# Optimization experiments

Measured on AMD Instinct MI355X. Metric: run time of the kernel, lower is better.

## Reference

```python
import jax, jax.numpy as jnp
import numpy as np

POOL = 7
IMG_H, IMG_W = 1024, 1024
EPS = 1e-3  # keras BatchNormalization default epsilon


def crop_and_resize(fmap, boxes, ph, pw):
    # TF tf.image.crop_and_resize (bilinear), box_indices == batch index of each roi.
    # fmap: [B,H,W,C], boxes: [B,N,4] normalized (y1,x1,y2,x2) -> [B,N,ph,pw,C]
    B, H, W, C = fmap.shape
    y1, x1, y2, x2 = jnp.split(boxes, 4, axis=-1)  # each [B,N,1]
    fy = jnp.arange(ph, dtype=boxes.dtype) / (ph - 1)
    fx = jnp.arange(pw, dtype=boxes.dtype) / (pw - 1)
    ys = (y1 + (y2 - y1) * fy) * (H - 1)  # [B,N,ph]
    xs = (x1 + (x2 - x1) * fx) * (W - 1)  # [B,N,pw]
    y0 = jnp.floor(ys)
    x0 = jnp.floor(xs)
    wy = (ys - y0)[:, :, :, None, None]  # [B,N,ph,1,1]
    wx = (xs - x0)[:, :, None, :, None]  # [B,N,1,pw,1]
    y0i = jnp.clip(y0.astype(jnp.int32), 0, H - 1)
    y1i = jnp.clip(y0i + 1, 0, H - 1)
    x0i = jnp.clip(x0.astype(jnp.int32), 0, W - 1)
    x1i = jnp.clip(x0i + 1, 0, W - 1)
    b = jnp.arange(B)[:, None, None, None]
    yi0 = y0i[:, :, :, None]; yi1 = y1i[:, :, :, None]   # [B,N,ph,1]
    xi0 = x0i[:, :, None, :]; xi1 = x1i[:, :, None, :]   # [B,N,1,pw]
    v00 = fmap[b, yi0, xi0]  # [B,N,ph,pw,C]
    v01 = fmap[b, yi0, xi1]
    v10 = fmap[b, yi1, xi0]
    v11 = fmap[b, yi1, xi1]
    top = v00 + (v01 - v00) * wx
    bot = v10 + (v11 - v10) * wx
    return top + (bot - top) * wy


def pyramid_roi_align(rois, fmaps, pool):
    # rois are stop-gradient in the original layer
    rois = jax.lax.stop_gradient(rois)
    y1, x1, y2, x2 = jnp.split(rois, 4, axis=-1)
    h = y2 - y1
    w = x2 - x1
    scale = 256.0 / np.sqrt(float(IMG_H * IMG_W))
    lvl = jnp.log2(jnp.maximum(jnp.sqrt(h * w), 1e-9) / scale)
    lvl = jnp.clip(4 + jnp.round(lvl).astype(jnp.int32), 2, 5)[..., 0]  # [B,N]
    B, N = rois.shape[:2]
    C = fmaps[0].shape[-1]
    out = jnp.zeros((B, N, pool, pool, C), fmaps[0].dtype)
    for i, fm in enumerate(fmaps):  # levels 2..5, fixed small loop
        sel = (lvl == i + 2)[:, :, None, None, None]
        out = jnp.where(sel, crop_and_resize(fm, rois, pool, pool), out)
    return out


def bn_train(x, gamma, beta):
    # keras BatchNorm with training=True: biased batch stats over all axes but channel
    m = x.mean(axis=(0, 1))
    v = x.var(axis=(0, 1))
    return (x - m) * jax.lax.rsqrt(v + EPS) * gamma + beta


def setup_inputs() -> dict:
    key = jax.random.key(0)
    ks = jax.random.split(key, 12)
    B, N, C, F = 2, 1000, 256, 1024
    # rois: valid boxes, sizes spanning all pyramid levels
    tl = jax.random.uniform(ks[0], (B, N, 2), jnp.float32, 0.0, 0.6)
    sz = jax.random.uniform(ks[1], (B, N, 2), jnp.float32, 0.02, 0.4)
    br = jnp.minimum(tl + sz, 1.0)
    rois = jnp.concatenate([tl[..., :1], tl[..., 1:], br[..., :1], br[..., 1:]], axis=-1)
    s = 0.02
    return {
        "rois": rois,
        "p2": jax.random.normal(ks[2], (B, 256, 256, C), jnp.float32),
        "p3": jax.random.normal(ks[3], (B, 128, 128, C), jnp.float32),
        "p4": jax.random.normal(ks[4], (B, 64, 64, C), jnp.float32),
        "p5": jax.random.normal(ks[5], (B, 32, 32, C), jnp.float32),
        "conv1_w": jax.random.normal(ks[6], (POOL, POOL, C, F), jnp.float32) * s,
        "conv1_b": jnp.zeros((F,), jnp.float32),
        "bn1_g": jnp.ones((F,), jnp.float32),
        "bn1_b": jnp.zeros((F,), jnp.float32),
        "conv2_w": jax.random.normal(ks[7], (F, F), jnp.float32) * s,
        "conv2_b": jnp.zeros((F,), jnp.float32),
        "bn2_g": jnp.ones((F,), jnp.float32),
        "bn2_b": jnp.zeros((F,), jnp.float32),
        "cls_w": jax.random.normal(ks[8], (F, 2), jnp.float32) * s,
        "cls_b": jnp.zeros((2,), jnp.float32),
        "delta_w": jax.random.normal(ks[9], (F, 8), jnp.float32) * s,
        "delta_b": jnp.zeros((8,), jnp.float32),
    }


def reference(rois, p2, p3, p4, p5, conv1_w, conv1_b, bn1_g, bn1_b,
              conv2_w, conv2_b, bn2_g, bn2_b, cls_w, cls_b, delta_w, delta_b):
    B, N = rois.shape[:2]
    n_classes = cls_w.shape[-1]
    pooled = pyramid_roi_align(rois, (p2, p3, p4, p5), POOL)  # [B,N,7,7,C]
    # Conv2D(F,(7,7),'valid') on a 7x7 input == full contraction over (h,w,c)
    x = jnp.einsum('bnhwc,hwcf->bnf', pooled, conv1_w) + conv1_b
    x = jax.nn.relu(bn_train(x, bn1_g, bn1_b))
    x = x @ conv2_w + conv2_b  # 1x1 conv == dense
    shared = jax.nn.relu(bn_train(x, bn2_g, bn2_b))  # [B,N,F]
    logits = shared @ cls_w + cls_b                  # [B,N,n_classes]
    probs = jax.nn.softmax(logits, axis=-1)
    deltas = (shared @ delta_w + delta_b).reshape(B, N, n_classes, 4)
    return logits, probs, deltas
```

## Files before the change

### kernel.cpp

```cpp
#include <hip/hip_runtime.h>
#include <hip/hip_bf16.h>

#define NB     2
#define NROI   1000
#define CIN    256
#define FDIM   1024
#define M_ROWS 2000
#define K1     12544
#define EPSBN  1e-3f
#define MN     (M_ROWS * FDIM)

typedef short bf16x8 __attribute__((ext_vector_type(8)));
typedef short bf16x4 __attribute__((ext_vector_type(4)));
typedef float f32x4  __attribute__((ext_vector_type(4)));

__device__ __forceinline__ void gld_lds16(const void* g, void* l) {
  __builtin_amdgcn_global_load_lds((const __attribute__((address_space(1))) char*)g,
                                   (__attribute__((address_space(3))) char*)l, 16, 0, 0);
}

__global__ __launch_bounds__(256) void transpose_to_bf16_v2(const float* __restrict__ W,
                                                            __hip_bfloat16* __restrict__ WT,
                                                            int K, int N) {
  __shared__ float tt[64][129];
  int k0 = blockIdx.x * 128, n0 = blockIdx.y * 64;
  int t = threadIdx.x;
  int r = t >> 4, cg = t & 15;
#pragma unroll
  for (int i = 0; i < 8; i++) {
    int row = i * 16 + r;
    f32x4 v = *(const f32x4*)(W + (size_t)(k0 + row) * N + n0 + cg * 4);
#pragma unroll
    for (int j = 0; j < 4; j++) tt[cg * 4 + j][row] = v[j];
  }
  __syncthreads();
  int n = t >> 4, g = t & 15;
#pragma unroll
  for (int pp = 0; pp < 4; pp++) {
    int nn = pp * 16 + n;
    bf16x8 o;
#pragma unroll
    for (int i = 0; i < 8; i++) {
      __hip_bfloat16 hh = __float2bfloat16(tt[nn][g * 8 + i]);
      o[i] = *reinterpret_cast<short*>(&hh);
    }
    *(bf16x8*)((short*)WT + (size_t)(n0 + nn) * K + k0 + g * 8) = o;
  }
}

__global__ __launch_bounds__(256) void roi_align_v2(const float* __restrict__ rois,
                                                    const float* __restrict__ p2,
                                                    const float* __restrict__ p3,
                                                    const float* __restrict__ p4,
                                                    const float* __restrict__ p5,
                                                    __hip_bfloat16* __restrict__ pooled) {
  int rn = blockIdx.x;
  int b = rn / NROI;

  const float* roi = rois + (size_t)rn * 4;
  float y1 = roi[0], x1 = roi[1], y2 = roi[2], x2 = roi[3];
  float h = y2 - y1, w = x2 - x1;
  float lvl = log2f(fmaxf(sqrtf(h * w), 1e-9f) * 4.0f);
  int li = 4 + (int)rintf(lvl);
  li = min(max(li, 2), 5) - 2;

  const float* fm; int H;
  switch (li) {
    case 0:  fm = p2; H = 256; break;
    case 1:  fm = p3; H = 128; break;
    case 2:  fm = p4; H = 64;  break;
    default: fm = p5; H = 32;  break;
  }
  int W = H;
  const float* fb = fm + (size_t)b * H * W * CIN;

  int lane = threadIdx.x & 63, wv = threadIdx.x >> 6;
  int c4 = lane * 4;

  for (int pos = wv; pos < 49; pos += 4) {
    int py = pos / 7, px = pos - py * 7;
    float fy = (float)py / 6.0f, fx = (float)px / 6.0f;
    float ys = (y1 + (y2 - y1) * fy) * (float)(H - 1);
    float xs = (x1 + (x2 - x1) * fx) * (float)(W - 1);
    float y0f = floorf(ys), x0f = floorf(xs);
    float wy = ys - y0f, wx = xs - x0f;
    int y0 = min(max((int)y0f, 0), H - 1);
    int x0 = min(max((int)x0f, 0), W - 1);
    int y1i = min(y0 + 1, H - 1);
    int x1i = min(x0 + 1, W - 1);

    f32x4 v00 = *(const f32x4*)(fb + ((size_t)y0 * W + x0) * CIN + c4);
    f32x4 v01 = *(const f32x4*)(fb + ((size_t)y0 * W + x1i) * CIN + c4);
    f32x4 v10 = *(const f32x4*)(fb + ((size_t)y1i * W + x0) * CIN + c4);
    f32x4 v11 = *(const f32x4*)(fb + ((size_t)y1i * W + x1i) * CIN + c4);

    f32x4 top = v00 + (v01 - v00) * wx;
    f32x4 bot = v10 + (v11 - v10) * wx;
    f32x4 val = top + (bot - top) * wy;

    bf16x4 o;
#pragma unroll
    for (int j = 0; j < 4; j++) {
      __hip_bfloat16 hh = __float2bfloat16(val[j]);
      o[j] = *reinterpret_cast<short*>(&hh);
    }
    *(bf16x4*)((short*)pooled + ((size_t)rn * 49 + pos) * CIN + c4) = o;
  }
}

template<int KSLICES>
__global__ __launch_bounds__(512) void gemm8w(const short* __restrict__ A,
                                              const short* __restrict__ BT,
                                              float* __restrict__ P,
                                              int M, int N, int K) {
  __shared__ short As[4 * 128 * 32];
  __shared__ short Bs[4 * 256 * 32];

  int nwg = gridDim.x;
  int bid = blockIdx.x;
  int cpx = nwg >> 3;
  int wg = (bid & 7) * cpx + (bid >> 3);

  int MT = (M + 127) >> 7;
  int NTn = N >> 8;
  int tiles = MT * NTn;
  int ks = wg / tiles;
  int rem = wg % tiles;
  int tm = rem % MT, tn = rem / MT;
  int m0 = tm * 128, n0 = tn * 256;
  int Kc = K / KSLICES;
  int NT = Kc >> 6;
  size_t kb = (size_t)ks * Kc;

  int tid = threadIdx.x;
  int lane = tid & 63, wid = tid >> 6;
  int wr = wid >> 2, wc = wid & 3;

  int srow = tid >> 2;
  int g = (tid & 3) ^ (srow & 3);
  const short* Agb  = A  + (size_t)min(m0 + srow, M - 1) * K + kb + g * 8;
  const short* Bgb0 = BT + (size_t)(n0 + srow) * K + kb + g * 8;
  const short* Bgb1 = Bgb0 + (size_t)128 * K;
  int aoff  = wid * 512;
  int boff0 = wid * 512;
  int boff1 = 4096 + wid * 512;

  int lr = lane & 15;
  int slotoff = ((lane >> 4) ^ (lane & 3)) * 8;
  const short* Ard = As + (wr * 64 + lr) * 32 + slotoff;
  const short* Brd = Bs + (wc * 64 + lr) * 32 + slotoff;

  f32x4 acc[4][4] = {};

#define STAGE(s) do {                                                        \
    int ts_ = (s) >> 1, kh_ = (s) & 1, b_ = ts_ & 1;                         \
    int ko_ = ts_ * 64 + kh_ * 32;                                           \
    short* Ad_ = (short*)As + (b_ * 2 + kh_) * 4096 + aoff;                  \
    short* Bd_ = (short*)Bs + (b_ * 2 + kh_) * 8192;                         \
    gld_lds16(Agb + ko_, Ad_);                                               \
    gld_lds16(Bgb0 + ko_, Bd_ + boff0);                                      \
    gld_lds16(Bgb1 + ko_, Bd_ + boff1);                                      \
  } while (0)

  STAGE(0); STAGE(1); STAGE(2);

  for (int t = 0; t < NT; ++t) {
    int b = t & 1;
#pragma unroll
    for (int kh = 0; kh < 2; ++kh) {
      __builtin_amdgcn_sched_barrier(0);
      if (t < NT - 1)      asm volatile("s_waitcnt vmcnt(6)" ::: "memory");
      else if (kh == 0)    asm volatile("s_waitcnt vmcnt(3)" ::: "memory");
      else                 asm volatile("s_waitcnt vmcnt(0)" ::: "memory");
      __builtin_amdgcn_s_barrier();
      __builtin_amdgcn_sched_barrier(0);

      const short* Ab = Ard + (b * 2 + kh) * 4096;
      const short* Bb = Brd + (b * 2 + kh) * 8192;
      bf16x8 af[4], bf_[4];
#pragma unroll
      for (int mi = 0; mi < 4; mi++) af[mi] = *(const bf16x8*)(Ab + mi * 512);
#pragma unroll
      for (int ni = 0; ni < 4; ni++) bf_[ni] = *(const bf16x8*)(Bb + ni * 512);

      if (kh == 0) { if (t + 1 < NT) STAGE(2 * t + 3); }
      else         { if (t + 2 < NT) STAGE(2 * t + 4); }

      __builtin_amdgcn_sched_barrier(0);
      asm volatile("s_waitcnt lgkmcnt(0)" ::: "memory");
      __builtin_amdgcn_sched_barrier(0);
      __builtin_amdgcn_s_setprio(1);
#pragma unroll
      for (int mi = 0; mi < 4; mi++)
#pragma unroll
        for (int ni = 0; ni < 4; ni++)
          acc[mi][ni] = __builtin_amdgcn_mfma_f32_16x16x32_bf16(af[mi], bf_[ni], acc[mi][ni], 0, 0, 0);
      __builtin_amdgcn_s_setprio(0);
    }
  }
#undef STAGE

  float* Pb = P + (size_t)ks * M * N;
  int crow = (lane >> 4) * 4, ccol = lane & 15;
#pragma unroll
  for (int mi = 0; mi < 4; mi++) {
    int rb = m0 + wr * 64 + mi * 16 + crow;
#pragma unroll
    for (int ni = 0; ni < 4; ni++) {
      int col = n0 + wc * 64 + ni * 16 + ccol;
#pragma unroll
      for (int r = 0; r < 4; r++) {
        int row = rb + r;
        if (row < M) Pb[(size_t)row * N + col] = acc[mi][ni][r];
      }
    }
  }
}

template<int KSLICES>
__global__ __launch_bounds__(256) void gemm128(const short* __restrict__ A,
                                               const short* __restrict__ BT,
                                               float* __restrict__ P,
                                               int M, int N, int K) {
  __shared__ short As[128 * 32];
  __shared__ short Bs[128 * 32];
  int nwg = gridDim.x;
  int bid = blockIdx.x;
  int cpx = nwg >> 3;
  int wg = (bid & 7) * cpx + (bid >> 3);

  int MT = (M + 127) >> 7;
  int NT = N >> 7;
  int ks   = wg / (MT * NT);
  int tile = wg % (MT * NT);
  int tm = tile % MT, tn = tile / MT;
  int m0 = tm * 128, n0 = tn * 128;
  int Kc = K / KSLICES;
  int kb = ks * Kc;

  int t = threadIdx.x;
  int lane = t & 63, wid = t >> 6;
  int wr = wid >> 1, wc = wid & 1;

  int q0 = wid * 64 + lane;
  int q1 = 256 + q0;
  int as0 = (q0 & 3) * 8, as1 = (q1 & 3) * 8;
  int ar0 = min(m0 + (q0 >> 2), M - 1);
  int ar1 = min(m0 + (q1 >> 2), M - 1);
  const short* Ag0 = A + (size_t)ar0 * K + kb + as0;
  const short* Ag1 = A + (size_t)ar1 * K + kb + as1;
  const short* Bg0 = BT + (size_t)(n0 + (q0 >> 2)) * K + kb + as0;
  const short* Bg1 = BT + (size_t)(n0 + (q1 >> 2)) * K + kb + as1;
  short* Asb0 = As + wid * 512;
  short* Asb1 = As + 2048 + wid * 512;
  short* Bsb0 = Bs + wid * 512;
  short* Bsb1 = Bs + 2048 + wid * 512;

  int lrow = lane & 15, lk = (lane >> 4) * 8;
  const short* Ar = As + (wr * 64 + lrow) * 32 + lk;
  const short* Br = Bs + (wc * 64 + lrow) * 32 + lk;

  f32x4 acc[4][4] = {};

  for (int k0 = 0; k0 < Kc; k0 += 32) {
    __syncthreads();
    gld_lds16(Ag0 + k0, Asb0);
    gld_lds16(Ag1 + k0, Asb1);
    gld_lds16(Bg0 + k0, Bsb0);
    gld_lds16(Bg1 + k0, Bsb1);
    __syncthreads();

    bf16x8 af[4], bfr[4];
#pragma unroll
    for (int i = 0; i < 4; i++) {
      af[i]  = *(const bf16x8*)(Ar + i * 512);
      bfr[i] = *(const bf16x8*)(Br + i * 512);
    }
#pragma unroll
    for (int mi = 0; mi < 4; mi++)
#pragma unroll
      for (int ni = 0; ni < 4; ni++)
        acc[mi][ni] = __builtin_amdgcn_mfma_f32_16x16x32_bf16(af[mi], bfr[ni], acc[mi][ni], 0, 0, 0);
  }

  float* Pb = P + (size_t)ks * M * N;
  int crow = (lane >> 4) * 4, ccol = lane & 15;
#pragma unroll
  for (int mi = 0; mi < 4; mi++) {
    int rb = m0 + wr * 64 + mi * 16 + crow;
#pragma unroll
    for (int ni = 0; ni < 4; ni++) {
      int col = n0 + wc * 64 + ni * 16 + ccol;
#pragma unroll
      for (int r = 0; r < 4; r++) {
        int row = rb + r;
        if (row < M) Pb[(size_t)row * N + col] = acc[mi][ni][r];
      }
    }
  }
}

__global__ void reduce_bias_stats(const float* __restrict__ P, const float* __restrict__ bias,
                                  float* __restrict__ X, float* __restrict__ stats,
                                  int M, int KS) {
  int t = threadIdx.x;
  int col = t * 4;
  f32x4 bv = *(const f32x4*)(bias + col);
  f32x4 s = {0, 0, 0, 0}, q = {0, 0, 0, 0};
  for (int r = blockIdx.x; r < M; r += gridDim.x) {
    size_t base = (size_t)r * FDIM + col;
    f32x4 v = *(const f32x4*)(P + base);
    for (int c = 1; c < KS; c++)
      v = v + *(const f32x4*)(P + (size_t)c * MN + base);
    v = v + bv;
    *(f32x4*)(X + base) = v;
    s = s + v;
    q = q + v * v;
  }
#pragma unroll
  for (int j = 0; j < 4; j++) {
    atomicAdd(&stats[col + j], s[j]);
    atomicAdd(&stats[FDIM + col + j], q[j]);
  }
}

__global__ void bn_norm_relu_bf16(const float* __restrict__ X, const float* __restrict__ stats,
                                  const float* __restrict__ g, const float* __restrict__ bta,
                                  __hip_bfloat16* __restrict__ obf, int M) {
  int idx = blockIdx.x * blockDim.x + threadIdx.x;
  if (idx >= M * FDIM) return;
  int f = idx & (FDIM - 1);
  float inv_m = 1.0f / (float)M;
  float mean = stats[f] * inv_m;
  float var = stats[FDIM + f] * inv_m - mean * mean;
  float xn = (X[idx] - mean) * rsqrtf(var + EPSBN) * g[f] + bta[f];
  obf[idx] = __float2bfloat16(fmaxf(xn, 0.0f));
}

__global__ void heads_bn(const float* __restrict__ X2, const float* __restrict__ stats,
                         const float* __restrict__ gg, const float* __restrict__ bb,
                         const float* __restrict__ cls_w, const float* __restrict__ cls_b,
                         const float* __restrict__ dw, const float* __restrict__ db,
                         float* __restrict__ out) {
  int row = blockIdx.x * 4 + (threadIdx.x >> 6);
  int lane = threadIdx.x & 63;
  if (row >= M_ROWS) return;
  const float* xrow = X2 + (size_t)row * FDIM;
  float inv_m = 1.0f / (float)M_ROWS;
  float a[10];
#pragma unroll
  for (int j = 0; j < 10; j++) a[j] = 0.0f;
  for (int k = lane; k < FDIM; k += 64) {
    float mean = stats[k] * inv_m;
    float var = stats[FDIM + k] * inv_m - mean * mean;
    float v = fmaxf((xrow[k] - mean) * rsqrtf(var + EPSBN) * gg[k] + bb[k], 0.0f);
    a[0] += v * cls_w[k * 2 + 0];
    a[1] += v * cls_w[k * 2 + 1];
#pragma unroll
    for (int j = 0; j < 8; j++) a[2 + j] += v * dw[k * 8 + j];
  }
#pragma unroll
  for (int j = 0; j < 10; j++)
    for (int o = 32; o > 0; o >>= 1) a[j] += __shfl_xor(a[j], o, 64);
  if (lane == 0) {
    float l0 = a[0] + cls_b[0], l1 = a[1] + cls_b[1];
    out[row * 2 + 0] = l0;
    out[row * 2 + 1] = l1;
    float mx = fmaxf(l0, l1);
    float e0 = expf(l0 - mx), e1 = expf(l1 - mx);
    float inv = 1.0f / (e0 + e1);
    out[4000 + row * 2 + 0] = e0 * inv;
    out[4000 + row * 2 + 1] = e1 * inv;
#pragma unroll
    for (int j = 0; j < 8; j++) out[8000 + row * 8 + j] = a[2 + j] + db[j];
  }
}

extern "C" void kernel_launch(void* const* d_in, const int* in_sizes, int n_in,
                              void* d_out, int out_size, void* d_ws, size_t ws_size,
                              hipStream_t stream) {
  const float* rois    = (const float*)d_in[0];
  const float* p2      = (const float*)d_in[1];
  const float* p3      = (const float*)d_in[2];
  const float* p4      = (const float*)d_in[3];
  const float* p5      = (const float*)d_in[4];
  const float* conv1_w = (const float*)d_in[5];
  const float* conv1_b = (const float*)d_in[6];
  const float* bn1_g   = (const float*)d_in[7];
  const float* bn1_b   = (const float*)d_in[8];
  const float* conv2_w = (const float*)d_in[9];
  const float* conv2_b = (const float*)d_in[10];
  const float* bn2_g   = (const float*)d_in[11];
  const float* bn2_b   = (const float*)d_in[12];
  const float* cls_w   = (const float*)d_in[13];
  const float* cls_b   = (const float*)d_in[14];
  const float* delta_w = (const float*)d_in[15];
  const float* delta_b = (const float*)d_in[16];
  float* out = (float*)d_out;

  char* ws = (char*)d_ws;
  size_t off = 0;
  __hip_bfloat16* pooled = (__hip_bfloat16*)(ws + off); off += (size_t)M_ROWS * K1 * 2;
  __hip_bfloat16* w1t    = (__hip_bfloat16*)(ws + off); off += (size_t)K1 * FDIM * 2;
  float* stats1          = (float*)(ws + off);          off += 2 * FDIM * 4;
  float* stats2          = (float*)(ws + off);          off += 2 * FDIM * 4;
  char*  Preg            = ws + off;                    off += (size_t)5 * MN * 4;
  float* part1           = (float*)Preg;
  float* x1              = (float*)Preg;
  __hip_bfloat16* x1n    = (__hip_bfloat16*)(Preg + (size_t)MN * 4);
  __hip_bfloat16* w2t    = (__hip_bfloat16*)(Preg + (size_t)2 * MN * 4);
  float* part2           = (float*)(Preg + (size_t)3 * MN * 4);
  float* x2              = part2;

  hipMemsetAsync(stats1, 0, 4 * FDIM * sizeof(float), stream);

  transpose_to_bf16_v2<<<dim3(K1 / 128, FDIM / 64), 256, 0, stream>>>(conv1_w, w1t, K1, FDIM);

  roi_align_v2<<<M_ROWS, 256, 0, stream>>>(rois, p2, p3, p4, p5, pooled);

  gemm8w<4><<<256, 512, 0, stream>>>((const short*)pooled, (const short*)w1t, part1,
                                     M_ROWS, FDIM, K1);
  reduce_bias_stats<<<256, 256, 0, stream>>>(part1, conv1_b, x1, stats1, M_ROWS, 4);

  bn_norm_relu_bf16<<<(MN + 255) / 256, 256, 0, stream>>>(x1, stats1, bn1_g, bn1_b, x1n, M_ROWS);

  transpose_to_bf16_v2<<<dim3(FDIM / 128, FDIM / 64), 256, 0, stream>>>(conv2_w, (__hip_bfloat16*)w2t, FDIM, FDIM);

  gemm128<2><<<256, 256, 0, stream>>>((const short*)x1n, (const short*)w2t, part2,
                                      M_ROWS, FDIM, FDIM);
  reduce_bias_stats<<<256, 256, 0, stream>>>(part2, conv2_b, x2, stats2, M_ROWS, 2);

  heads_bn<<<(M_ROWS + 3) / 4, 256, 0, stream>>>(x2, stats2, bn2_g, bn2_b,
                                                 cls_w, cls_b, delta_w, delta_b, out);

  (void)in_sizes; (void)n_in; (void)out_size; (void)ws_size;
}
```

Before: 217.1 us.

## Fuse prep kernels into one launch and reuse gemm8w for second GEMM

```diff
diff --git a/kernel.cpp b/kernel.cpp
--- a/kernel.cpp
+++ b/kernel.cpp
@@ -19,92 +19,112 @@
                                    (__attribute__((address_space(3))) char*)l, 16, 0, 0);
 }
 
-__global__ __launch_bounds__(256) void transpose_to_bf16_v2(const float* __restrict__ W,
-                                                            __hip_bfloat16* __restrict__ WT,
-                                                            int K, int N) {
-  __shared__ float tt[64][129];
-  int k0 = blockIdx.x * 128, n0 = blockIdx.y * 64;
+__global__ __launch_bounds__(256) void prep_kernel(
+    const float* __restrict__ rois,
+    const float* __restrict__ p2, const float* __restrict__ p3,
+    const float* __restrict__ p4, const float* __restrict__ p5,
+    __hip_bfloat16* __restrict__ pooled,
+    const float* __restrict__ conv1_w, __hip_bfloat16* __restrict__ w1t,
+    const float* __restrict__ conv2_w, __hip_bfloat16* __restrict__ w2t,
+    float* __restrict__ stats) {
+  __shared__ float tt[64][65];
+  int idx = blockIdx.x;
   int t = threadIdx.x;
-  int r = t >> 4, cg = t & 15;
-#pragma unroll
-  for (int i = 0; i < 8; i++) {
-    int row = i * 16 + r;
-    f32x4 v = *(const f32x4*)(W + (size_t)(k0 + row) * N + n0 + cg * 4);
-#pragma unroll
-    for (int j = 0; j < 4; j++) tt[cg * 4 + j][row] = v[j];
+
+  if (idx == 0) {
+#pragma unroll
+    for (int i = 0; i < 4; i++)
+      ((f32x4*)stats)[t + i * 256] = f32x4{0, 0, 0, 0};
+    return;
+  }
+
+  if (idx < 1 + M_ROWS) {
+    int rn = idx - 1;
+    int b = rn / NROI;
+
+    const float* roi = rois + (size_t)rn * 4;
+    float y1 = roi[0], x1 = roi[1], y2 = roi[2], x2 = roi[3];
+    float h = y2 - y1, w = x2 - x1;
+    float lvl = log2f(fmaxf(sqrtf(h * w), 1e-9f) * 4.0f);
+    int li = 4 + (int)rintf(lvl);
+    li = min(max(li, 2), 5) - 2;
+
+    const float* fm; int H;
+    switch (li) {
+      case 0:  fm = p2; H = 256; break;
+      case 1:  fm = p3; H = 128; break;
+      case 2:  fm = p4; H = 64;  break;
+      default: fm = p5; H = 32;  break;
+    }
+    int W = H;
+    const float* fb = fm + (size_t)b * H * W * CIN;
+
+    int lane = t & 63, wv = t >> 6;
+    int c4 = lane * 4;
+
+    for (int pos = wv; pos < 49; pos += 4) {
+      int py = pos / 7, px = pos - py * 7;
+      float fy = (float)py / 6.0f, fx = (float)px / 6.0f;
+      float ys = (y1 + (y2 - y1) * fy) * (float)(H - 1);
+      float xs = (x1 + (x2 - x1) * fx) * (float)(W - 1);
+      float y0f = floorf(ys), x0f = floorf(xs);
+      float wy = ys - y0f, wx = xs - x0f;
+      int y0 = min(max((int)y0f, 0), H - 1);
+      int x0 = min(max((int)x0f, 0), W - 1);
+      int y1i = min(y0 + 1, H - 1);
+      int x1i = min(x0 + 1, W - 1);
+
+      f32x4 v00 = *(const f32x4*)(fb + ((size_t)y0 * W + x0) * CIN + c4);
+      f32x4 v01 = *(const f32x4*)(fb + ((size_t)y0 * W + x1i) * CIN + c4);
+      f32x4 v10 = *(const f32x4*)(fb + ((size_t)y1i * W + x0) * CIN + c4);
+      f32x4 v11 = *(const f32x4*)(fb + ((size_t)y1i * W + x1i) * CIN + c4);
+
+      f32x4 top = v00 + (v01 - v00) * wx;
+      f32x4 bot = v10 + (v11 - v10) * wx;
+      f32x4 val = top + (bot - top) * wy;
+
+      bf16x4 o;
+#pragma unroll
+      for (int j = 0; j < 4; j++) {
+        __hip_bfloat16 hh = __float2bfloat16(val[j]);
+        o[j] = *reinterpret_cast<short*>(&hh);
+      }
+      *(bf16x4*)((short*)pooled + ((size_t)rn * 49 + pos) * CIN + c4) = o;
+    }
+    return;
+  }
+
+  const float* W; short* WT; int K, N, bx, by;
+  if (idx < 1 + M_ROWS + 3136) {
+    int wk = idx - (1 + M_ROWS);
+    W = conv1_w; WT = (short*)w1t; K = K1; N = FDIM;
+    bx = wk % 196; by = wk / 196;
+  } else {
+    int wk = idx - (1 + M_ROWS + 3136);
+    W = conv2_w; WT = (short*)w2t; K = FDIM; N = FDIM;
+    bx = wk % 16; by = wk / 16;
+  }
+  int k0 = bx * 64, n0 = by * 64;
+  int r = t >> 2, c = t & 3;
+#pragma unroll
+  for (int i = 0; i < 4; i++) {
+    int cg = c * 4 + i;
+    f32x4 v = *(const f32x4*)(W + (size_t)(k0 + r) * N + n0 + cg * 4);
+#pragma unroll
+    for (int j = 0; j < 4; j++) tt[cg * 4 + j][r] = v[j];
   }
   __syncthreads();
-  int n = t >> 4, g = t & 15;
-#pragma unroll
-  for (int pp = 0; pp < 4; pp++) {
-    int nn = pp * 16 + n;
+  int n = t >> 2, g = t & 3;
+#pragma unroll
+  for (int i = 0; i < 2; i++) {
+    int seg = g * 2 + i;
     bf16x8 o;
 #pragma unroll
-    for (int i = 0; i < 8; i++) {
-      __hip_bfloat16 hh = __float2bfloat16(tt[nn][g * 8 + i]);
-      o[i] = *reinterpret_cast<short*>(&hh);
-    }
-    *(bf16x8*)((short*)WT + (size_t)(n0 + nn) * K + k0 + g * 8) = o;
-  }
-}
-
-__global__ __launch_bounds__(256) void roi_align_v2(const float* __restrict__ rois,
-                                                    const float* __restrict__ p2,
-                                                    const float* __restrict__ p3,
-                                                    const float* __restrict__ p4,
-                                                    const float* __restrict__ p5,
-                                                    __hip_bfloat16* __restrict__ pooled) {
-  int rn = blockIdx.x;
-  int b = rn / NROI;
-
-  const float* roi = rois + (size_t)rn * 4;
-  float y1 = roi[0], x1 = roi[1], y2 = roi[2], x2 = roi[3];
-  float h = y2 - y1, w = x2 - x1;
-  float lvl = log2f(fmaxf(sqrtf(h * w), 1e-9f) * 4.0f);
-  int li = 4 + (int)rintf(lvl);
-  li = min(max(li, 2), 5) - 2;
-
-  const float* fm; int H;
-  switch (li) {
-    case 0:  fm = p2; H = 256; break;
-    case 1:  fm = p3; H = 128; break;
-    case 2:  fm = p4; H = 64;  break;
-    default: fm = p5; H = 32;  break;
-  }
-  int W = H;
-  const float* fb = fm + (size_t)b * H * W * CIN;
-
-  int lane = threadIdx.x & 63, wv = threadIdx.x >> 6;
-  int c4 = lane * 4;
-
-  for (int pos = wv; pos < 49; pos += 4) {
-    int py = pos / 7, px = pos - py * 7;
-    float fy = (float)py / 6.0f, fx = (float)px / 6.0f;
-    float ys = (y1 + (y2 - y1) * fy) * (float)(H - 1);
-    float xs = (x1 + (x2 - x1) * fx) * (float)(W - 1);
-    float y0f = floorf(ys), x0f = floorf(xs);
-    float wy = ys - y0f, wx = xs - x0f;
-    int y0 = min(max((int)y0f, 0), H - 1);
-    int x0 = min(max((int)x0f, 0), W - 1);
-    int y1i = min(y0 + 1, H - 1);
-    int x1i = min(x0 + 1, W - 1);
-
-    f32x4 v00 = *(const f32x4*)(fb + ((size_t)y0 * W + x0) * CIN + c4);
-    f32x4 v01 = *(const f32x4*)(fb + ((size_t)y0 * W + x1i) * CIN + c4);
-    f32x4 v10 = *(const f32x4*)(fb + ((size_t)y1i * W + x0) * CIN + c4);
-    f32x4 v11 = *(const f32x4*)(fb + ((size_t)y1i * W + x1i) * CIN + c4);
-
-    f32x4 top = v00 + (v01 - v00) * wx;
-    f32x4 bot = v10 + (v11 - v10) * wx;
-    f32x4 val = top + (bot - top) * wy;
-
-    bf16x4 o;
-#pragma unroll
-    for (int j = 0; j < 4; j++) {
-      __hip_bfloat16 hh = __float2bfloat16(val[j]);
+    for (int j = 0; j < 8; j++) {
+      __hip_bfloat16 hh = __float2bfloat16(tt[n][seg * 8 + j]);
       o[j] = *reinterpret_cast<short*>(&hh);
     }
-    *(bf16x4*)((short*)pooled + ((size_t)rn * 49 + pos) * CIN + c4) = o;
+    *(bf16x8*)(WT + (size_t)(n0 + n) * K + k0 + seg * 8) = o;
   }
 }
 
@@ -199,89 +219,6 @@
     }
   }
 #undef STAGE
-
-  float* Pb = P + (size_t)ks * M * N;
-  int crow = (lane >> 4) * 4, ccol = lane & 15;
-#pragma unroll
-  for (int mi = 0; mi < 4; mi++) {
-    int rb = m0 + wr * 64 + mi * 16 + crow;
-#pragma unroll
-    for (int ni = 0; ni < 4; ni++) {
-      int col = n0 + wc * 64 + ni * 16 + ccol;
-#pragma unroll
-      for (int r = 0; r < 4; r++) {
-        int row = rb + r;
-        if (row < M) Pb[(size_t)row * N + col] = acc[mi][ni][r];
-      }
-    }
-  }
-}
-
-template<int KSLICES>
-__global__ __launch_bounds__(256) void gemm128(const short* __restrict__ A,
-                                               const short* __restrict__ BT,
-                                               float* __restrict__ P,
-                                               int M, int N, int K) {
-  __shared__ short As[128 * 32];
-  __shared__ short Bs[128 * 32];
-  int nwg = gridDim.x;
-  int bid = blockIdx.x;
-  int cpx = nwg >> 3;
-  int wg = (bid & 7) * cpx + (bid >> 3);
-
-  int MT = (M + 127) >> 7;
-  int NT = N >> 7;
-  int ks   = wg / (MT * NT);
-  int tile = wg % (MT * NT);
-  int tm = tile % MT, tn = tile / MT;
-  int m0 = tm * 128, n0 = tn * 128;
-  int Kc = K / KSLICES;
-  int kb = ks * Kc;
-
-  int t = threadIdx.x;
-  int lane = t & 63, wid = t >> 6;
-  int wr = wid >> 1, wc = wid & 1;
-
-  int q0 = wid * 64 + lane;
-  int q1 = 256 + q0;
-  int as0 = (q0 & 3) * 8, as1 = (q1 & 3) * 8;
-  int ar0 = min(m0 + (q0 >> 2), M - 1);
-  int ar1 = min(m0 + (q1 >> 2), M - 1);
-  const short* Ag0 = A + (size_t)ar0 * K + kb + as0;
-  const short* Ag1 = A + (size_t)ar1 * K + kb + as1;
-  const short* Bg0 = BT + (size_t)(n0 + (q0 >> 2)) * K + kb + as0;
-  const short* Bg1 = BT + (size_t)(n0 + (q1 >> 2)) * K + kb + as1;
-  short* Asb0 = As + wid * 512;
-  short* Asb1 = As + 2048 + wid * 512;
-  short* Bsb0 = Bs + wid * 512;
-  short* Bsb1 = Bs + 2048 + wid * 512;
-
-  int lrow = lane & 15, lk = (lane >> 4) * 8;
-  const short* Ar = As + (wr * 64 + lrow) * 32 + lk;
-  const short* Br = Bs + (wc * 64 + lrow) * 32 + lk;
-
-  f32x4 acc[4][4] = {};
-
-  for (int k0 = 0; k0 < Kc; k0 += 32) {
-    __syncthreads();
-    gld_lds16(Ag0 + k0, Asb0);
-    gld_lds16(Ag1 + k0, Asb1);
-    gld_lds16(Bg0 + k0, Bsb0);
-    gld_lds16(Bg1 + k0, Bsb1);
-    __syncthreads();
-
-    bf16x8 af[4], bfr[4];
-#pragma unroll
-    for (int i = 0; i < 4; i++) {
-      af[i]  = *(const bf16x8*)(Ar + i * 512);
-      bfr[i] = *(const bf16x8*)(Br + i * 512);
-    }
-#pragma unroll
-    for (int mi = 0; mi < 4; mi++)
-#pragma unroll
-      for (int ni = 0; ni < 4; ni++)
-        acc[mi][ni] = __builtin_amdgcn_mfma_f32_16x16x32_bf16(af[mi], bfr[ni], acc[mi][ni], 0, 0, 0);
-  }
 
   float* Pb = P + (size_t)ks * M * N;
   int crow = (lane >> 4) * 4, ccol = lane & 15;
@@ -402,33 +339,28 @@
   size_t off = 0;
   __hip_bfloat16* pooled = (__hip_bfloat16*)(ws + off); off += (size_t)M_ROWS * K1 * 2;
   __hip_bfloat16* w1t    = (__hip_bfloat16*)(ws + off); off += (size_t)K1 * FDIM * 2;
+  __hip_bfloat16* w2t    = (__hip_bfloat16*)(ws + off); off += (size_t)FDIM * FDIM * 2;
   float* stats1          = (float*)(ws + off);          off += 2 * FDIM * 4;
   float* stats2          = (float*)(ws + off);          off += 2 * FDIM * 4;
-  char*  Preg            = ws + off;                    off += (size_t)5 * MN * 4;
-  float* part1           = (float*)Preg;
-  float* x1              = (float*)Preg;
-  __hip_bfloat16* x1n    = (__hip_bfloat16*)(Preg + (size_t)MN * 4);
-  __hip_bfloat16* w2t    = (__hip_bfloat16*)(Preg + (size_t)2 * MN * 4);
-  float* part2           = (float*)(Preg + (size_t)3 * MN * 4);
-  float* x2              = part2;
-
-  hipMemsetAsync(stats1, 0, 4 * FDIM * sizeof(float), stream);
-
-  transpose_to_bf16_v2<<<dim3(K1 / 128, FDIM / 64), 256, 0, stream>>>(conv1_w, w1t, K1, FDIM);
-
-  roi_align_v2<<<M_ROWS, 256, 0, stream>>>(rois, p2, p3, p4, p5, pooled);
+  char*  Preg            = ws + off;                    off += (size_t)4 * MN * 4;
+  float* part1        = (float*)Preg;
+  float* x1           = (float*)Preg;
+  __hip_bfloat16* x1n = (__hip_bfloat16*)pooled;
+  float* part2        = (float*)Preg;
+  float* x2           = (float*)Preg;
+
+  prep_kernel<<<1 + M_ROWS + 3136 + 256, 256, 0, stream>>>(
+      rois, p2, p3, p4, p5, pooled, conv1_w, w1t, conv2_w, w2t, stats1);
 
   gemm8w<4><<<256, 512, 0, stream>>>((const short*)pooled, (const short*)w1t, part1,
                                      M_ROWS, FDIM, K1);
   reduce_bias_stats<<<256, 256, 0, stream>>>(part1, conv1_b, x1, stats1, M_ROWS, 4);
 
-  bn_norm_relu_bf16<<<(MN + 255) / 256, 256, 0, stream>>>(x1, stats1, bn1_g, bn1_b, x1n, M_ROWS);
-
-  transpose_to_bf16_v2<<<dim3(FDIM / 128, FDIM / 64), 256, 0, stream>>>(conv2_w, (__hip_bfloat16*)w2t, FDIM, FDIM);
-
-  gemm128<2><<<256, 256, 0, stream>>>((const short*)x1n, (const short*)w2t, part2,
-                                      M_ROWS, FDIM, FDIM);
-  reduce_bias_stats<<<256, 256, 0, stream>>>(part2, conv2_b, x2, stats2, M_ROWS, 2);
+  bn_norm_relu_bf16<<<MN / 256, 256, 0, stream>>>(x1, stats1, bn1_g, bn1_b, x1n, M_ROWS);
+
+  gemm8w<4><<<256, 512, 0, stream>>>((const short*)x1n, (const short*)w2t, part2,
+                                     M_ROWS, FDIM, FDIM);
+  reduce_bias_stats<<<256, 256, 0, stream>>>(part2, conv2_b, x2, stats2, M_ROWS, 4);
 
   heads_bn<<<(M_ROWS + 3) / 4, 256, 0, stream>>>(x2, stats2, bn2_g, bn2_b,
                                                  cls_w, cls_b, delta_w, delta_b, out);
```

After: 210.8 us. 2.9% less time.
